# Kernel optimization log

Measured on AMD Instinct MI355X. Metric: run time of the kernel, lower is better.

Reference implementation:

```python
import jax, jax.numpy as jnp
import numpy as np

SCALE_BASE = 512
EPS = 1e-5


def _xpos_factors(seq_len, head_dim):
    half = head_dim // 2
    # xpos scale vector: ((arange(0, hd, 2) + 0.4*hd) / (1.4*hd)) ** (pos / scale_base)
    s = (jnp.arange(0, head_dim, 2, dtype=jnp.float32) + 0.4 * head_dim) / (1.4 * head_dim)
    pos = jnp.arange(seq_len, dtype=jnp.float32)
    scale = s[None, :] ** (pos[:, None] / SCALE_BASE)          # (S, half)
    inv_freq = 1.0 / (10000.0 ** (jnp.arange(half, dtype=jnp.float32) / half))
    ang = pos[:, None] * inv_freq[None, :]                     # (S, half)
    return jnp.sin(ang), jnp.cos(ang), scale


def _dup_interleave(m):
    # (S, half) -> (S, head_dim): each column duplicated, interleaved
    return jnp.repeat(m, 2, axis=-1)


def _rotate_every_two(x):
    x1, x2 = x[..., ::2], x[..., 1::2]
    return jnp.stack((-x2, x1), axis=-1).reshape(x.shape)


def _apply_xpos(x, sin, cos, scale):
    sinf = _dup_interleave(sin * scale)                        # (S, hd)
    cosf = _dup_interleave(cos * scale)
    return x * cosf + _rotate_every_two(x) * sinf


def _decay_mask(gammas, seq_len, chunk_size):
    # D[h, i, j] = gamma_h ** |i - j| if j < ((i // chunk) + 1) * chunk else 0
    i = jnp.arange(seq_len)[:, None]
    j = jnp.arange(seq_len)[None, :]
    allowed = j < ((i // chunk_size) + 1) * chunk_size         # (S, S)
    expo = jnp.abs(i - j).astype(jnp.float32)
    D = gammas[:, None, None] ** expo[None]                    # (H, S, S)
    return jnp.where(allowed[None], D, 0.0)


def setup_inputs() -> dict:
    key = jax.random.key(0)
    B, S, hidden, H, hd, chunk = 4, 2048, 512, 8, 64, 64
    ks = jax.random.split(key, 6)
    return {
        "X": jax.random.normal(ks[0], (B, S, hidden), dtype=jnp.float32),
        "W_Q": jax.random.normal(ks[1], (H, hidden, hd), dtype=jnp.float32) / hidden,
        "W_K": jax.random.normal(ks[2], (H, hidden, hd), dtype=jnp.float32) / hidden,
        "W_V": jax.random.normal(ks[3], (H, hidden, hd), dtype=jnp.float32) / hidden,
        "W_G": jax.random.normal(ks[4], (hidden, H * hd), dtype=jnp.float32) / hidden,
        "W_O": jax.random.normal(ks[5], (H * hd, hidden), dtype=jnp.float32) / hidden,
        "gn_weight": jnp.ones((H * hd,), dtype=jnp.float32),
        "gn_bias": jnp.zeros((H * hd,), dtype=jnp.float32),
        "chunk_size": chunk,
    }


def reference(X, W_Q, W_K, W_V, W_G, W_O, gn_weight, gn_bias, chunk_size):
    B, S, hidden = X.shape
    H, _, hd = W_Q.shape
    # RetNet multi-scale decay rates
    gammas = 1.0 - jnp.exp(
        jnp.linspace(jnp.log(jnp.float32(1 / 32)), jnp.log(jnp.float32(1 / 512)), H)
    )
    D = _decay_mask(gammas, S, chunk_size)                     # (H, S, S)

    # per-head projections: n = heads
    Q = jnp.einsum("bsh,nhd->bnsd", X, W_Q)
    K = jnp.einsum("bsh,nhd->bnsd", X, W_K)
    V = jnp.einsum("bsh,nhd->bnsd", X, W_V)

    sin, cos, scale = _xpos_factors(S, hd)
    Q = _apply_xpos(Q, sin, cos, scale)                        # broadcast (S,hd) over (B,H,S,hd)
    K = _apply_xpos(K, sin, cos, 1.0 / scale)                  # downscale

    scores = jnp.einsum("bnsd,bntd->bnst", Q, K) * D[None]     # (B,H,S,S)
    Yh = jnp.einsum("bnst,bntd->bnsd", scores, V)              # (B,H,S,hd)

    # concat heads -> (B,S,H*hd), GroupNorm(heads) per token (stats over each head's hd channels)
    Y = Yh.transpose(0, 2, 1, 3)                               # (B,S,H,hd)
    mu = Y.mean(-1, keepdims=True)
    var = Y.var(-1, keepdims=True)
    Yn = (Y - mu) / jnp.sqrt(var + EPS)
    Yn = Yn.reshape(B, S, H * hd) * gn_weight + gn_bias

    gate = jax.nn.silu(X @ W_G)                                # swish(X W_G)
    return (gate * Yn) @ W_O
```

## Files before the change

### kernel.cpp

```cpp
#include <hip/hip_runtime.h>

#define B_   4
#define S_   2048
#define HID  512
#define H_   8
#define HD   64

typedef __attribute__((ext_vector_type(8))) short bf16x8;
typedef __attribute__((ext_vector_type(4))) float f32x4;

#define MFMA16(a, b, c) __builtin_amdgcn_mfma_f32_16x16x32_bf16(a, b, c, 0, 0, 0)

#define GAMMA_L0   (-3.4657359027997265f)
#define GAMMA_STEP (-0.3960841031771116f)

__device__ __forceinline__ void async16(const void* g, void* l) {
    __builtin_amdgcn_global_load_lds(
        (const __attribute__((address_space(1))) void*)g,
        (__attribute__((address_space(3))) void*)l, 16, 0, 0);
}

__device__ __forceinline__ unsigned short f2bf(float x) {
    unsigned u = __float_as_uint(x);
    return (unsigned short)((u + 0x7fffu + ((u >> 16) & 1u)) >> 16);
}
__device__ __forceinline__ float bfs2f(short s) {
    return __uint_as_float(((unsigned)(unsigned short)s) << 16);
}
__device__ __forceinline__ unsigned packbf(float lo, float hi) {
    return (unsigned)f2bf(lo) | ((unsigned)f2bf(hi) << 16);
}

__global__ __launch_bounds__(256) void prep(
    const float* __restrict__ X,
    const float* __restrict__ Wq, const float* __restrict__ Wk,
    const float* __restrict__ Wv, const float* __restrict__ Wg,
    const float* __restrict__ Wo,
    short* __restrict__ Xb,
    short* __restrict__ WqT, short* __restrict__ WkT, short* __restrict__ WvT,
    short* __restrict__ WgT, short* __restrict__ WoT,
    float4* __restrict__ Lut)
{
    __shared__ float T[64][65];
    const int bid = blockIdx.x, t = threadIdx.x;

    if (bid < 2048) {
        size_t i = ((size_t)bid * 256 + t) * 8;
        float4 a = *(const float4*)&X[i];
        float4 b = *(const float4*)&X[i + 4];
        union { int4 v; unsigned short s[8]; } u;
        u.s[0] = f2bf(a.x); u.s[1] = f2bf(a.y); u.s[2] = f2bf(a.z); u.s[3] = f2bf(a.w);
        u.s[4] = f2bf(b.x); u.s[5] = f2bf(b.y); u.s[6] = f2bf(b.z); u.s[7] = f2bf(b.w);
        *(int4*)&Xb[i] = u.v;
        return;
    }
    if (bid >= 2368) {
        int idx = (bid - 2368) * 256 + t;
        int s = idx >> 5, k = idx & 31;
        float invf = exp2f(-0.41524101186092035f * (float)k);
        float ang  = (float)s * invf;
        float sn = sinf(ang), cs = cosf(ang);
        float sk = ((float)(2 * k) + 25.6f) / 89.6f;
        float sc = exp2f(log2f(sk) * (float)s * (1.0f / 512.0f));
        Lut[idx] = (float4){cs * sc, sn * sc, cs / sc, sn / sc};
        return;
    }

    const int wb = bid - 2048;
    const float* ip; short* op; int ild;
    if (wb < 192) {
        int which = wb >> 6, rem = wb & 63, h = rem >> 3, kt = rem & 7;
        const float* src = which == 0 ? Wq : which == 1 ? Wk : Wv;
        short* dst       = which == 0 ? WqT : which == 1 ? WkT : WvT;
        ip = src + ((size_t)h * 512 + kt * 64) * 64;
        ild = 64;
        op = dst + (size_t)(h * 64) * 512 + kt * 64;
    } else {
        int rem = wb - 192, which = rem >> 6, r3 = rem & 63, nt = r3 >> 3, kt = r3 & 7;
        const float* src = which ? Wo : Wg;
        short* dst       = which ? WoT : WgT;
        ip = src + (size_t)(kt * 64) * 512 + nt * 64;
        ild = 512;
        op = dst + (size_t)(nt * 64) * 512 + kt * 64;
    }
    {
        int r = t >> 2, c0 = (t & 3) * 16;
        #pragma unroll
        for (int e = 0; e < 4; ++e) {
            float4 f = *(const float4*)&ip[(size_t)r * ild + c0 + e * 4];
            T[r][c0 + e*4 + 0] = f.x; T[r][c0 + e*4 + 1] = f.y;
            T[r][c0 + e*4 + 2] = f.z; T[r][c0 + e*4 + 3] = f.w;
        }
    }
    __syncthreads();
    {
        int cc = t >> 2, r0 = (t & 3) * 16;
        short* orow = op + (size_t)cc * 512;
        #pragma unroll
        for (int ii = 0; ii < 8; ++ii) {
            int lo = f2bf(T[r0 + 2*ii][cc]);
            int hi = f2bf(T[r0 + 2*ii + 1][cc]);
            *(int*)(orow + r0 + 2*ii) = (lo & 0xffff) | (hi << 16);
        }
    }
}

__device__ __forceinline__ void stage64k(const short* __restrict__ Ag,
                                         const short* __restrict__ Bg,
                                         int k0, short* As, short* Bs, int tid)
{
    #pragma unroll
    for (int j = 0; j < 2; ++j) {
        int idx = j * 256 + tid;
        int row = idx >> 3, c8 = (idx & 7) ^ (row & 7);
        async16(Ag + (size_t)row * 512 + k0 + c8 * 8, As + idx * 8);
    }
    #pragma unroll
    for (int j = 0; j < 4; ++j) {
        int idx = j * 256 + tid;
        int row = idx >> 3, c8 = (idx & 7) ^ (row & 7);
        async16(Bg + (size_t)row * 512 + k0 + c8 * 8, Bs + idx * 8);
    }
}

__device__ __forceinline__ void gemm_core64(const short* __restrict__ Ag,
                                            const short* __restrict__ Bg,
                                            short* SM, f32x4 (&acc)[2][4])
{
    const int tid = threadIdx.x;
    const int L = tid & 63, quad = L >> 4, l16 = L & 15;
    const int w = tid >> 6;
    const int wrow = (w >> 1) * 32, wcol = (w & 1) * 64;
    short* As = SM;
    short* Bs = SM + 4096;

    for (int k0 = 0; k0 < 512; k0 += 64) {
        stage64k(Ag, Bg, k0, As, Bs, tid);
        __syncthreads();
        #pragma unroll
        for (int ks = 0; ks < 2; ++ks) {
            bf16x8 af[2], bfr[4];
            #pragma unroll
            for (int a = 0; a < 2; ++a) {
                int m = wrow + a * 16 + l16;
                af[a] = *(const bf16x8*)&As[m * 64 + ((quad + 4 * ks) ^ (m & 7)) * 8];
            }
            #pragma unroll
            for (int b = 0; b < 4; ++b) {
                int n = wcol + b * 16 + l16;
                bfr[b] = *(const bf16x8*)&Bs[n * 64 + ((quad + 4 * ks) ^ (n & 7)) * 8];
            }
            #pragma unroll
            for (int a = 0; a < 2; ++a)
                #pragma unroll
                for (int b = 0; b < 4; ++b)
                    acc[a][b] = MFMA16(af[a], bfr[b], acc[a][b]);
        }
        __syncthreads();
    }
}

__global__ __launch_bounds__(256) void fused_gemm(
    const short* __restrict__ Xb, const short* __restrict__ WT,
    const float4* __restrict__ Lut,
    short* __restrict__ Qb, short* __restrict__ Kb, short* __restrict__ Vb,
    short* __restrict__ Gb)
{
    __shared__ short SM[12288];
    const int by = blockIdx.x;
    const int bx = blockIdx.y;

    f32x4 acc[2][4];
    #pragma unroll
    for (int a = 0; a < 2; ++a)
        #pragma unroll
        for (int b = 0; b < 4; ++b) acc[a][b] = (f32x4){0.f, 0.f, 0.f, 0.f};

    gemm_core64(Xb + (size_t)by * 64 * 512,
                WT + (size_t)bx * 128 * 512, SM, acc);

    const int tid = threadIdx.x, L = tid & 63, quad = L >> 4, l16 = L & 15;
    const int w = tid >> 6, wrow = (w >> 1) * 32, wcol = (w & 1) * 64;
    const int zone = bx >> 2;
    short* Out = (zone == 0) ? Qb : (zone == 1) ? Kb : Vb;

    #pragma unroll
    for (int b = 0; b < 4; ++b) {
        int ncol = (bx & 3) * 128 + wcol + b * 16 + l16;
        int d = ncol & 63, k = d >> 1;
        int colE = wcol + b * 16 + (l16 & ~1);
        #pragma unroll
        for (int a = 0; a < 2; ++a) {
            #pragma unroll
            for (int r = 0; r < 4; ++r) {
                int m = by * 64 + wrow + a * 16 + quad * 4 + r;
                int s = m & 2047;
                float v = acc[a][b][r];
                unsigned word;
                if (zone == 3) {
                    float g = v / (1.0f + __expf(-v));
                    float part = __shfl_xor(g, 1);
                    word = packbf(g, part);
                } else {
                    float part = __shfl_xor(v, 1);
                    float e = (d & 1) ? part : v;
                    float o = (d & 1) ? v : part;
                    if (zone == 2) {
                        word = packbf(e, o);
                    } else {
                        float4 f = Lut[s * 32 + k];
                        float cs = (zone == 0) ? f.x : f.z;
                        float sn = (zone == 0) ? f.y : f.w;
                        word = packbf(e * cs - o * sn, o * cs + e * sn);
                    }
                }
                if (!(l16 & 1))
                    *(int*)&SM[(wrow + a * 16 + quad * 4 + r) * 136 + colE] = word;
            }
        }
    }
    __syncthreads();
    #pragma unroll
    for (int j = 0; j < 4; ++j) {
        int idx = j * 256 + tid;
        int row = idx >> 4, c0 = (idx & 15) * 8;
        int m = by * 64 + row;
        int n = (bx & 3) * 128 + c0;
        if (zone == 3) {
            *(int4*)&Gb[(size_t)m * 512 + n] = *(const int4*)&SM[row * 136 + c0];
        } else {
            int bb = m >> 11, s = m & 2047;
            int h = n >> 6, d = n & 63;
            *(int4*)&Out[(((size_t)bb * 8 + h) * 2048 + s) * 64 + d] =
                *(const int4*)&SM[row * 136 + c0];
        }
    }
}

__global__ __launch_bounds__(256) void out_gemm(
    const short* __restrict__ Zb, const short* __restrict__ WoT,
    float* __restrict__ Of)
{
    __shared__ short SM[12288];
    const int by = blockIdx.x;
    const int bx = blockIdx.y;

    f32x4 acc[2][4];
    #pragma unroll
    for (int a = 0; a < 2; ++a)
        #pragma unroll
        for (int b = 0; b < 4; ++b) acc[a][b] = (f32x4){0.f, 0.f, 0.f, 0.f};

    gemm_core64(Zb + (size_t)by * 64 * 512,
                WoT + (size_t)bx * 128 * 512, SM, acc);

    const int tid = threadIdx.x, L = tid & 63, quad = L >> 4, l16 = L & 15;
    const int w = tid >> 6, wrow = (w >> 1) * 32, wcol = (w & 1) * 64;
    #pragma unroll
    for (int b = 0; b < 4; ++b) {
        int ncol = bx * 128 + wcol + b * 16 + l16;
        #pragma unroll
        for (int a = 0; a < 2; ++a)
            #pragma unroll
            for (int r = 0; r < 4; ++r) {
                int m = by * 64 + wrow + a * 16 + quad * 4 + r;
                Of[(size_t)m * 512 + ncol] = acc[a][b][r];
            }
    }
}

__global__ __launch_bounds__(256) void ret_g(
    const short* __restrict__ Kb, const short* __restrict__ Vb,
    short* __restrict__ Gt)
{
    __shared__ short Kt[64 * 72];
    __shared__ short Vt[64 * 72];
    const int tid = threadIdx.x, L = tid & 63, quad = L >> 4, l16 = L & 15;
    const int w = tid >> 6;
    const int c = blockIdx.x, bn = blockIdx.y, hh = bn & 7;

    float gamma = 1.0f - expf(GAMMA_L0 + GAMMA_STEP * (float)hh);
    float lg = log2f(gamma);

    {
        const short* kg = Kb + ((size_t)bn * 2048 + c * 64 + L) * 64 + w * 16;
        const short* vg = Vb + ((size_t)bn * 2048 + c * 64 + L) * 64 + w * 16;
        float wgt = exp2f(lg * (float)(64 - L));
        int4 k0 = *(const int4*)kg; int4 k1 = *(const int4*)(kg + 8);
        int4 v0 = *(const int4*)vg; int4 v1 = *(const int4*)(vg + 8);
        short* kt = Kt + L; short* vt = Vt + L;
        #pragma unroll
        for (int q = 0; q < 4; ++q) {
            int uk = ((const int*)&k0)[q];
            kt[(w*16 + 2*q)     * 72] = (short)f2bf(bfs2f((short)uk) * wgt);
            kt[(w*16 + 2*q + 1) * 72] = (short)f2bf(bfs2f((short)(uk >> 16)) * wgt);
            int uv = ((const int*)&v0)[q];
            vt[(w*16 + 2*q)     * 72] = (short)uv;
            vt[(w*16 + 2*q + 1) * 72] = (short)(uv >> 16);
        }
        #pragma unroll
        for (int q = 0; q < 4; ++q) {
            int uk = ((const int*)&k1)[q];
            kt[(w*16 + 8 + 2*q) * 72] = (short)f2bf(bfs2f((short)uk) * wgt);
            kt[(w*16 + 9 + 2*q) * 72] = (short)f2bf(bfs2f((short)(uk >> 16)) * wgt);
            int uv = ((const int*)&v1)[q];
            vt[(w*16 + 8 + 2*q) * 72] = (short)uv;
            vt[(w*16 + 9 + 2*q) * 72] = (short)(uv >> 16);
        }
    }
    __syncthreads();

    bf16x8 a0 = *(const bf16x8*)&Vt[(w * 16 + l16) * 72 + quad * 8];
    bf16x8 a1 = *(const bf16x8*)&Vt[(w * 16 + l16) * 72 + 32 + quad * 8];
    short* Gp = Gt + ((size_t)bn * 32 + c) * 4096;
    #pragma unroll
    for (int b = 0; b < 4; ++b) {
        bf16x8 b0 = *(const bf16x8*)&Kt[(b * 16 + l16) * 72 + quad * 8];
        bf16x8 b1 = *(const bf16x8*)&Kt[(b * 16 + l16) * 72 + 32 + quad * 8];
        f32x4 acc = (f32x4){0.f, 0.f, 0.f, 0.f};
        acc = MFMA16(a0, b0, acc);
        acc = MFMA16(a1, b1, acc);
        #pragma unroll
        for (int r = 0; r < 4; ++r) {
            float v = acc[r];
            float part = __shfl_xor(v, 1);
            unsigned word = packbf(v, part);
            if (!(l16 & 1))
                *(int*)&Gp[(w*16 + quad*4 + r) * 64 + b * 16 + (l16 & ~1)] = word;
        }
    }
}

__global__ __launch_bounds__(256) void ret_scan(short* __restrict__ GM)
{
    const int tid = threadIdx.x, seg = blockIdx.x, bn = blockIdx.y, hh = bn & 7;
    float gamma = 1.0f - expf(GAMMA_L0 + GAMMA_STEP * (float)hh);
    float g64 = exp2f(log2f(gamma) * 64.0f);

    size_t base = (size_t)bn * 32 * 4096 + seg * 1024 + tid * 4;
    float m0 = 0.f, m1 = 0.f, m2 = 0.f, m3 = 0.f;
    #pragma unroll 4
    for (int c = 0; c < 32; ++c) {
        int2* p = (int2*)&GM[base + (size_t)c * 4096];
        int2 g = *p;
        *p = make_int2((int)packbf(m0, m1), (int)packbf(m2, m3));
        m0 = g64 * m0 + bfs2f((short)g.x);
        m1 = g64 * m1 + bfs2f((short)(g.x >> 16));
        m2 = g64 * m2 + bfs2f((short)g.y);
        m3 = g64 * m3 + bfs2f((short)(g.y >> 16));
    }
}

__global__ __launch_bounds__(256) void ret_main(
    const short* __restrict__ Qb, const short* __restrict__ Kb,
    const short* __restrict__ Vb, const short* __restrict__ Mb,
    const short* __restrict__ Gb,
    const float* __restrict__ gw, const float* __restrict__ gb,
    short* __restrict__ Zb)
{
    __shared__ short Qs[4096];
    __shared__ short Ks[4096];
    __shared__ short Ms[4096];
    __shared__ short Vt[64 * 72];
    __shared__ short Pw[4][16 * 72];

    const int tid = threadIdx.x, L = tid & 63, quad = L >> 4, l16 = L & 15;
    const int w = tid >> 6;
    const int c = blockIdx.x, bn = blockIdx.y, hh = bn & 7, bb = bn >> 3;

    float gamma = 1.0f - expf(GAMMA_L0 + GAMMA_STEP * (float)hh);
    float lg = log2f(gamma);

    float Dabs[4][4];
    #pragma unroll
    for (int b = 0; b < 4; ++b)
        #pragma unroll
        for (int r = 0; r < 4; ++r) {
            int dlt = (w * 16 + quad * 4 + r) - (b * 16 + l16);
            Dabs[b][r] = exp2f(lg * fabsf((float)dlt));
        }
    float gq[4];
    #pragma unroll
    for (int r = 0; r < 4; ++r)
        gq[r] = exp2f(lg * (float)(w * 16 + quad * 4 + r));

    {
        const short* qg = Qb + ((size_t)bn * 2048 + c * 64 + w * 16 + (L >> 2)) * 64 + (L & 3) * 8;
        async16(qg,      Qs + w * 512 + L * 8);
        async16(qg + 32, Qs + 2048 + w * 512 + L * 8);
        const short* kg = Kb + ((size_t)bn * 2048 + c * 64 + w * 16 + (L >> 2)) * 64 + (L & 3) * 8;
        async16(kg,      Ks + w * 512 + L * 8);
        async16(kg + 32, Ks + 2048 + w * 512 + L * 8);
        const short* mg = Mb + ((size_t)bn * 32 + c) * 4096 + (w * 16 + (L >> 2)) * 64 + (L & 3) * 8;
        async16(mg,      Ms + w * 512 + L * 8);
        async16(mg + 32, Ms + 2048 + w * 512 + L * 8);
    }
    {
        const short* vg = Vb + ((size_t)bn * 2048 + c * 64 + L) * 64 + w * 16;
        int4 v0 = *(const int4*)vg;
        int4 v1 = *(const int4*)(vg + 8);
        short* vt = Vt + L;
        #pragma unroll
        for (int q = 0; q < 4; ++q) {
            int u = ((const int*)&v0)[q];
            vt[(w*16 + 2*q)     * 72] = (short)u;
            vt[(w*16 + 2*q + 1) * 72] = (short)(u >> 16);
        }
        #pragma unroll
        for (int q = 0; q < 4; ++q) {
            int u = ((const int*)&v1)[q];
            vt[(w*16 + 8 + 2*q) * 72] = (short)u;
            vt[(w*16 + 9 + 2*q) * 72] = (short)(u >> 16);
        }
    }
    __syncthreads();

    bf16x8 aQ0 = *(const bf16x8*)&Qs[(w * 16 + l16) * 32 + quad * 8];
    bf16x8 aQ1 = *(const bf16x8*)&Qs[2048 + (w * 16 + l16) * 32 + quad * 8];
    f32x4 accM[4];
    #pragma unroll
    for (int b = 0; b < 4; ++b) {
        bf16x8 k0 = *(const bf16x8*)&Ks[(b * 16 + l16) * 32 + quad * 8];
        bf16x8 k1 = *(const bf16x8*)&Ks[2048 + (b * 16 + l16) * 32 + quad * 8];
        f32x4 S = (f32x4){0.f, 0.f, 0.f, 0.f};
        S = MFMA16(aQ0, k0, S);
        S = MFMA16(aQ1, k1, S);
        #pragma unroll
        for (int r = 0; r < 4; ++r)
            Pw[w][(quad * 4 + r) * 72 + b * 16 + l16] = (short)f2bf(S[r] * Dabs[b][r]);

        bf16x8 m0 = *(const bf16x8*)&Ms[(b * 16 + l16) * 32 + quad * 8];
        bf16x8 m1 = *(const bf16x8*)&Ms[2048 + (b * 16 + l16) * 32 + quad * 8];
        f32x4 Mv = (f32x4){0.f, 0.f, 0.f, 0.f};
        Mv = MFMA16(aQ0, m0, Mv);
        Mv = MFMA16(aQ1, m1, Mv);
        accM[b] = Mv;
    }

    bf16x8 aP0 = *(const bf16x8*)&Pw[w][l16 * 72 + quad * 8];
    bf16x8 aP1 = *(const bf16x8*)&Pw[w][l16 * 72 + 32 + quad * 8];
    f32x4 Y4[4];
    #pragma unroll
    for (int b2 = 0; b2 < 4; ++b2) {
        bf16x8 v0f = *(const bf16x8*)&Vt[(b2 * 16 + l16) * 72 + quad * 8];
        bf16x8 v1f = *(const bf16x8*)&Vt[(b2 * 16 + l16) * 72 + 32 + quad * 8];
        f32x4 yv = (f32x4){0.f, 0.f, 0.f, 0.f};
        yv = MFMA16(aP0, v0f, yv);
        yv = MFMA16(aP1, v1f, yv);
        #pragma unroll
        for (int r = 0; r < 4; ++r)
            Y4[b2][r] = yv[r] + gq[r] * accM[b2][r];
    }

    #pragma unroll
    for (int r = 0; r < 4; ++r) {
        float s1 = 0.f, s2 = 0.f;
        #pragma unroll
        for (int b2 = 0; b2 < 4; ++b2) {
            float v = Y4[b2][r];
            s1 += v; s2 += v * v;
        }
        #pragma unroll
        for (int off = 1; off < 16; off <<= 1) {
            s1 += __shfl_xor(s1, off);
            s2 += __shfl_xor(s2, off);
        }
        float mu = s1 * (1.0f / 64.0f);
        float var = s2 * (1.0f / 64.0f) - mu * mu;
        float rstd = rsqrtf(var + 1e-5f);

        int il = w * 16 + quad * 4 + r;
        size_t row = (size_t)bb * 2048 + c * 64 + il;
        #pragma unroll
        for (int b2 = 0; b2 < 4; ++b2) {
            int j = hh * 64 + b2 * 16 + l16;
            float yn = (Y4[b2][r] - mu) * rstd * gw[j] + gb[j];
            float z = bfs2f(Gb[row * 512 + j]) * yn;
            float part = __shfl_xor(z, 1);
            if (!(l16 & 1))
                *(int*)&Zb[row * 512 + hh * 64 + b2 * 16 + (l16 & ~1)] = packbf(z, part);
        }
    }
}

extern "C" void kernel_launch(void* const* d_in, const int* in_sizes, int n_in,
                              void* d_out, int out_size, void* d_ws, size_t ws_size,
                              hipStream_t stream)
{
    const float* X  = (const float*)d_in[0];
    const float* Wq = (const float*)d_in[1];
    const float* Wk = (const float*)d_in[2];
    const float* Wv = (const float*)d_in[3];
    const float* Wg = (const float*)d_in[4];
    const float* Wo = (const float*)d_in[5];
    const float* gw = (const float*)d_in[6];
    const float* gb = (const float*)d_in[7];

    char* ws = (char*)d_ws;
    short* Xb  = (short*)ws;
    short* WqT = (short*)(ws + 8388608);
    short* WkT = WqT + 262144;
    short* WvT = WkT + 262144;
    short* WgT = WvT + 262144;
    short* WoT = WgT + 262144;
    short* Qb  = (short*)(ws + 11010048);
    short* Kb  = Qb + 4194304;
    short* Vb  = Kb + 4194304;
    float4* Lut = (float4*)(ws + 36175872);
    short* GM  = (short*)(ws + 37224448);
    short* Zb  = (short*)(ws + 45613056);
    short* Gb  = (short*)(ws + 54001664);

    prep<<<2624, 256, 0, stream>>>(X, Wq, Wk, Wv, Wg, Wo,
                                   Xb, WqT, WkT, WvT, WgT, WoT, Lut);
    fused_gemm<<<dim3(128, 16), 256, 0, stream>>>(Xb, WqT, Lut, Qb, Kb, Vb, Gb);
    ret_g<<<dim3(32, 32), 256, 0, stream>>>(Kb, Vb, GM);
    ret_scan<<<dim3(4, 32), 256, 0, stream>>>(GM);
    ret_main<<<dim3(32, 32), 256, 0, stream>>>(Qb, Kb, Vb, GM, Gb, gw, gb, Zb);
    out_gemm<<<dim3(128, 4), 256, 0, stream>>>(Zb, WoT, (float*)d_out);
}
```

Baseline: 164.6 us.

## Fuse chunk-state GEMM with decay scan and retile output GEMM to 64x64

Merges the per-chunk K^T V state kernel and the separate decay scan into one kernel. Each block walks all chunks of a batch-head, carrying the running state in registers and prefetching the next chunk's K/V. This removes a launch and a global round-trip of the intermediate states, at the cost of far fewer blocks and a serial loop. The output projection is also retiled to 64x64 tiles with its own XOR-swizzled async loads, doubling the grid size.

```diff
diff --git a/kernel.cpp b/kernel.cpp
--- a/kernel.cpp
+++ b/kernel.cpp
@@ -241,24 +241,59 @@
     const short* __restrict__ Zb, const short* __restrict__ WoT,
     float* __restrict__ Of)
 {
-    __shared__ short SM[12288];
+    __shared__ short SM[8192];
     const int by = blockIdx.x;
     const int bx = blockIdx.y;
 
-    f32x4 acc[2][4];
+    f32x4 acc[2][2];
     #pragma unroll
     for (int a = 0; a < 2; ++a)
         #pragma unroll
-        for (int b = 0; b < 4; ++b) acc[a][b] = (f32x4){0.f, 0.f, 0.f, 0.f};
-
-    gemm_core64(Zb + (size_t)by * 64 * 512,
-                WoT + (size_t)bx * 128 * 512, SM, acc);
-
-    const int tid = threadIdx.x, L = tid & 63, quad = L >> 4, l16 = L & 15;
-    const int w = tid >> 6, wrow = (w >> 1) * 32, wcol = (w & 1) * 64;
-    #pragma unroll
-    for (int b = 0; b < 4; ++b) {
-        int ncol = bx * 128 + wcol + b * 16 + l16;
+        for (int b = 0; b < 2; ++b) acc[a][b] = (f32x4){0.f, 0.f, 0.f, 0.f};
+
+    const int tid = threadIdx.x;
+    const int L = tid & 63, quad = L >> 4, l16 = L & 15;
+    const int w = tid >> 6;
+    const int wrow = (w >> 1) * 32, wcol = (w & 1) * 32;
+    const short* Ag = Zb + (size_t)by * 64 * 512;
+    const short* Bg = WoT + (size_t)bx * 64 * 512;
+    short* As = SM;
+    short* Bs = SM + 4096;
+
+    for (int k0 = 0; k0 < 512; k0 += 64) {
+        #pragma unroll
+        for (int j = 0; j < 2; ++j) {
+            int idx = j * 256 + tid;
+            int row = idx >> 3, c8 = (idx & 7) ^ (row & 7);
+            async16(Ag + (size_t)row * 512 + k0 + c8 * 8, As + idx * 8);
+            async16(Bg + (size_t)row * 512 + k0 + c8 * 8, Bs + idx * 8);
+        }
+        __syncthreads();
+        #pragma unroll
+        for (int ks = 0; ks < 2; ++ks) {
+            bf16x8 af[2], bfr[2];
+            #pragma unroll
+            for (int a = 0; a < 2; ++a) {
+                int m = wrow + a * 16 + l16;
+                af[a] = *(const bf16x8*)&As[m * 64 + ((quad + 4 * ks) ^ (m & 7)) * 8];
+            }
+            #pragma unroll
+            for (int b = 0; b < 2; ++b) {
+                int n = wcol + b * 16 + l16;
+                bfr[b] = *(const bf16x8*)&Bs[n * 64 + ((quad + 4 * ks) ^ (n & 7)) * 8];
+            }
+            #pragma unroll
+            for (int a = 0; a < 2; ++a)
+                #pragma unroll
+                for (int b = 0; b < 2; ++b)
+                    acc[a][b] = MFMA16(af[a], bfr[b], acc[a][b]);
+        }
+        __syncthreads();
+    }
+
+    #pragma unroll
+    for (int b = 0; b < 2; ++b) {
+        int ncol = bx * 64 + wcol + b * 16 + l16;
         #pragma unroll
         for (int a = 0; a < 2; ++a)
             #pragma unroll
@@ -269,85 +304,89 @@
     }
 }
 
-__global__ __launch_bounds__(256) void ret_g(
+__global__ __launch_bounds__(256) void ret_gm(
     const short* __restrict__ Kb, const short* __restrict__ Vb,
-    short* __restrict__ Gt)
+    short* __restrict__ Mb)
 {
     __shared__ short Kt[64 * 72];
     __shared__ short Vt[64 * 72];
     const int tid = threadIdx.x, L = tid & 63, quad = L >> 4, l16 = L & 15;
     const int w = tid >> 6;
-    const int c = blockIdx.x, bn = blockIdx.y, hh = bn & 7;
+    const int bn = blockIdx.x, hh = bn & 7;
 
     float gamma = 1.0f - expf(GAMMA_L0 + GAMMA_STEP * (float)hh);
     float lg = log2f(gamma);
-
-    {
-        const short* kg = Kb + ((size_t)bn * 2048 + c * 64 + L) * 64 + w * 16;
-        const short* vg = Vb + ((size_t)bn * 2048 + c * 64 + L) * 64 + w * 16;
-        float wgt = exp2f(lg * (float)(64 - L));
-        int4 k0 = *(const int4*)kg; int4 k1 = *(const int4*)(kg + 8);
-        int4 v0 = *(const int4*)vg; int4 v1 = *(const int4*)(vg + 8);
-        short* kt = Kt + L; short* vt = Vt + L;
-        #pragma unroll
-        for (int q = 0; q < 4; ++q) {
-            int uk = ((const int*)&k0)[q];
-            kt[(w*16 + 2*q)     * 72] = (short)f2bf(bfs2f((short)uk) * wgt);
-            kt[(w*16 + 2*q + 1) * 72] = (short)f2bf(bfs2f((short)(uk >> 16)) * wgt);
-            int uv = ((const int*)&v0)[q];
-            vt[(w*16 + 2*q)     * 72] = (short)uv;
-            vt[(w*16 + 2*q + 1) * 72] = (short)(uv >> 16);
-        }
-        #pragma unroll
-        for (int q = 0; q < 4; ++q) {
-            int uk = ((const int*)&k1)[q];
-            kt[(w*16 + 8 + 2*q) * 72] = (short)f2bf(bfs2f((short)uk) * wgt);
-            kt[(w*16 + 9 + 2*q) * 72] = (short)f2bf(bfs2f((short)(uk >> 16)) * wgt);
-            int uv = ((const int*)&v1)[q];
-            vt[(w*16 + 8 + 2*q) * 72] = (short)uv;
-            vt[(w*16 + 9 + 2*q) * 72] = (short)(uv >> 16);
-        }
-    }
-    __syncthreads();
-
-    bf16x8 a0 = *(const bf16x8*)&Vt[(w * 16 + l16) * 72 + quad * 8];
-    bf16x8 a1 = *(const bf16x8*)&Vt[(w * 16 + l16) * 72 + 32 + quad * 8];
-    short* Gp = Gt + ((size_t)bn * 32 + c) * 4096;
-    #pragma unroll
-    for (int b = 0; b < 4; ++b) {
-        bf16x8 b0 = *(const bf16x8*)&Kt[(b * 16 + l16) * 72 + quad * 8];
-        bf16x8 b1 = *(const bf16x8*)&Kt[(b * 16 + l16) * 72 + 32 + quad * 8];
-        f32x4 acc = (f32x4){0.f, 0.f, 0.f, 0.f};
-        acc = MFMA16(a0, b0, acc);
-        acc = MFMA16(a1, b1, acc);
-        #pragma unroll
-        for (int r = 0; r < 4; ++r) {
-            float v = acc[r];
-            float part = __shfl_xor(v, 1);
-            unsigned word = packbf(v, part);
-            if (!(l16 & 1))
-                *(int*)&Gp[(w*16 + quad*4 + r) * 64 + b * 16 + (l16 & ~1)] = word;
-        }
-    }
-}
-
-__global__ __launch_bounds__(256) void ret_scan(short* __restrict__ GM)
-{
-    const int tid = threadIdx.x, seg = blockIdx.x, bn = blockIdx.y, hh = bn & 7;
-    float gamma = 1.0f - expf(GAMMA_L0 + GAMMA_STEP * (float)hh);
-    float g64 = exp2f(log2f(gamma) * 64.0f);
-
-    size_t base = (size_t)bn * 32 * 4096 + seg * 1024 + tid * 4;
-    float m0 = 0.f, m1 = 0.f, m2 = 0.f, m3 = 0.f;
-    #pragma unroll 4
+    float g64 = exp2f(lg * 64.0f);
+    float wgt = exp2f(lg * (float)(64 - L));
+
+    const short* Kbase = Kb + ((size_t)bn * 2048 + L) * 64 + w * 16;
+    const short* Vbase = Vb + ((size_t)bn * 2048 + L) * 64 + w * 16;
+
+    f32x4 M[4];
+    #pragma unroll
+    for (int b = 0; b < 4; ++b) M[b] = (f32x4){0.f, 0.f, 0.f, 0.f};
+
+    int4 k0 = *(const int4*)Kbase;      int4 k1 = *(const int4*)(Kbase + 8);
+    int4 v0 = *(const int4*)Vbase;      int4 v1 = *(const int4*)(Vbase + 8);
+
     for (int c = 0; c < 32; ++c) {
-        int2* p = (int2*)&GM[base + (size_t)c * 4096];
-        int2 g = *p;
-        *p = make_int2((int)packbf(m0, m1), (int)packbf(m2, m3));
-        m0 = g64 * m0 + bfs2f((short)g.x);
-        m1 = g64 * m1 + bfs2f((short)(g.x >> 16));
-        m2 = g64 * m2 + bfs2f((short)g.y);
-        m3 = g64 * m3 + bfs2f((short)(g.y >> 16));
+        __syncthreads();
+        {
+            short* kt = Kt + L; short* vt = Vt + L;
+            #pragma unroll
+            for (int q = 0; q < 4; ++q) {
+                int uk = ((const int*)&k0)[q];
+                kt[(w*16 + 2*q)     * 72] = (short)f2bf(bfs2f((short)uk) * wgt);
+                kt[(w*16 + 2*q + 1) * 72] = (short)f2bf(bfs2f((short)(uk >> 16)) * wgt);
+                int uv = ((const int*)&v0)[q];
+                vt[(w*16 + 2*q)     * 72] = (short)uv;
+                vt[(w*16 + 2*q + 1) * 72] = (short)(uv >> 16);
+            }
+            #pragma unroll
+            for (int q = 0; q < 4; ++q) {
+                int uk = ((const int*)&k1)[q];
+                kt[(w*16 + 8 + 2*q) * 72] = (short)f2bf(bfs2f((short)uk) * wgt);
+                kt[(w*16 + 9 + 2*q) * 72] = (short)f2bf(bfs2f((short)(uk >> 16)) * wgt);
+                int uv = ((const int*)&v1)[q];
+                vt[(w*16 + 8 + 2*q) * 72] = (short)uv;
+                vt[(w*16 + 9 + 2*q) * 72] = (short)(uv >> 16);
+            }
+        }
+        __syncthreads();
+
+        if (c + 1 < 32) {
+            const short* kn = Kbase + (size_t)(c + 1) * 64 * 64;
+            const short* vn = Vbase + (size_t)(c + 1) * 64 * 64;
+            k0 = *(const int4*)kn; k1 = *(const int4*)(kn + 8);
+            v0 = *(const int4*)vn; v1 = *(const int4*)(vn + 8);
+        }
+
+        short* Mp = Mb + ((size_t)bn * 32 + c) * 4096;
+        #pragma unroll
+        for (int b = 0; b < 4; ++b) {
+            #pragma unroll
+            for (int r = 0; r < 4; ++r) {
+                float v = M[b][r];
+                float part = __shfl_xor(v, 1);
+                unsigned word = packbf(v, part);
+                if (!(l16 & 1))
+                    *(int*)&Mp[(w*16 + quad*4 + r) * 64 + b * 16 + (l16 & ~1)] = word;
+            }
+        }
+
+        bf16x8 a0 = *(const bf16x8*)&Vt[(w * 16 + l16) * 72 + quad * 8];
+        bf16x8 a1 = *(const bf16x8*)&Vt[(w * 16 + l16) * 72 + 32 + quad * 8];
+        #pragma unroll
+        for (int b = 0; b < 4; ++b) {
+            bf16x8 b0 = *(const bf16x8*)&Kt[(b * 16 + l16) * 72 + quad * 8];
+            bf16x8 b1 = *(const bf16x8*)&Kt[(b * 16 + l16) * 72 + 32 + quad * 8];
+            f32x4 accG = (f32x4){0.f, 0.f, 0.f, 0.f};
+            accG = MFMA16(a0, b0, accG);
+            accG = MFMA16(a1, b1, accG);
+            #pragma unroll
+            for (int r = 0; r < 4; ++r)
+                M[b][r] = g64 * M[b][r] + accG[r];
+        }
     }
 }
 
@@ -514,8 +553,7 @@
     prep<<<2624, 256, 0, stream>>>(X, Wq, Wk, Wv, Wg, Wo,
                                    Xb, WqT, WkT, WvT, WgT, WoT, Lut);
     fused_gemm<<<dim3(128, 16), 256, 0, stream>>>(Xb, WqT, Lut, Qb, Kb, Vb, Gb);
-    ret_g<<<dim3(32, 32), 256, 0, stream>>>(Kb, Vb, GM);
-    ret_scan<<<dim3(4, 32), 256, 0, stream>>>(GM);
+    ret_gm<<<dim3(32), 256, 0, stream>>>(Kb, Vb, GM);
     ret_main<<<dim3(32, 32), 256, 0, stream>>>(Qb, Kb, Vb, GM, Gb, gw, gb, Zb);
-    out_gemm<<<dim3(128, 4), 256, 0, stream>>>(Zb, WoT, (float*)d_out);
-}
+    out_gemm<<<dim3(128, 8), 256, 0, stream>>>(Zb, WoT, (float*)d_out);
+}
```

Measured after the change: 196.2 us. 1.19x slower.
